# Kernel tuning notes

Hardware: AMD Instinct MI355X
Metric: run time of the kernel (lower is better)

Reference implementation:

```python
import jax, jax.numpy as jnp
import numpy as np

T, B, D = 256, 256, 512
H, DK = 8, 64          # num_heads, d_kv; inner_dim = H*DK = 512
NUM_GROUPS = 16


def setup_inputs() -> dict:
    key = jax.random.key(0)
    ks = jax.random.split(key, 6)
    hidden_states = jax.random.normal(ks[0], (T, B, D), dtype=jnp.float32)
    # sorted group ids over the batch axis (what _infer_group_ids_from_mask recovers)
    group_ids = jnp.sort(jax.random.randint(ks[1], (B,), 0, NUM_GROUPS, dtype=jnp.int32))
    scale = 1.0 / np.sqrt(D)
    Wq = jax.random.normal(ks[2], (D, H * DK), dtype=jnp.float32) * scale
    Wk = jax.random.normal(ks[3], (D, H * DK), dtype=jnp.float32) * scale
    Wv = jax.random.normal(ks[4], (D, H * DK), dtype=jnp.float32) * scale
    Wo = jax.random.normal(ks[5], (H * DK, D), dtype=jnp.float32) * scale
    return {"hidden_states": hidden_states, "group_ids": group_ids,
            "Wq": Wq, "Wk": Wk, "Wv": Wv, "Wo": Wo}


def reference(hidden_states, group_ids, Wq, Wk, Wv, Wo):
    # Group-restricted self-attention along the batch axis, per time step & head.
    # Equivalent to the block-sparse MiniFlash kernel: entries attend only to
    # batch entries with the same group id.
    t, b, d = hidden_states.shape
    q = (hidden_states @ Wq).reshape(t, b, H, DK)
    k = (hidden_states @ Wk).reshape(t, b, H, DK)
    v = (hidden_states @ Wv).reshape(t, b, H, DK)
    sm_scale = 1.0 / np.sqrt(DK)
    # scores: [T, H, B, B] over the batch axis
    scores = jnp.einsum("tihd,tjhd->thij", q, k) * sm_scale
    allowed = group_ids[:, None] == group_ids[None, :]          # [B, B]
    neg = jnp.finfo(scores.dtype).min
    scores = jnp.where(allowed[None, None, :, :], scores, neg)
    attn = jax.nn.softmax(scores, axis=-1)
    out = jnp.einsum("thij,tjhd->tihd", attn, v).reshape(t, b, H * DK)
    return out @ Wo
```

## Files before the change

### kernel.cpp

```cpp
#include <hip/hip_runtime.h>
#include <hip/hip_bf16.h>

typedef __attribute__((ext_vector_type(8))) short short8;
typedef __attribute__((ext_vector_type(4))) short short4v;
typedef __attribute__((ext_vector_type(4))) float f32x4;

#define MFMA16(a, b, c) __builtin_amdgcn_mfma_f32_16x16x32_bf16(a, b, c, 0, 0, 0)

__device__ __forceinline__ unsigned short f2bf(float f) {
    __hip_bfloat16 h = __float2bfloat16(f);
    union { __hip_bfloat16 h; unsigned short u; } v;
    v.h = h;
    return v.u;
}

__device__ __forceinline__ short8 pack8(float4 a, float4 b) {
    short8 p;
    p[0] = (short)f2bf(a.x); p[1] = (short)f2bf(a.y);
    p[2] = (short)f2bf(a.z); p[3] = (short)f2bf(a.w);
    p[4] = (short)f2bf(b.x); p[5] = (short)f2bf(b.y);
    p[6] = (short)f2bf(b.z); p[7] = (short)f2bf(b.w);
    return p;
}

__global__ __launch_bounds__(256) void wprep(
    const float* __restrict__ Wq, const float* __restrict__ Wk,
    const float* __restrict__ Wv, const float* __restrict__ Wo,
    unsigned short* __restrict__ wt)
{
    __shared__ float tile[64][65];
    const int bid = blockIdx.x;
    const int m = bid >> 6, tb = bid & 63;
    const int kr = (tb >> 3) << 6, nc = (tb & 7) << 6;
    const float* W = (m == 0) ? Wq : (m == 1) ? Wk : (m == 2) ? Wv : Wo;
    const int tid = threadIdx.x;
    for (int i = tid; i < 4096; i += 256)
        tile[i >> 6][i & 63] = W[(size_t)(kr + (i >> 6)) * 512 + nc + (i & 63)];
    __syncthreads();
    unsigned short* dst = wt + (size_t)m * 262144;
    for (int i = tid; i < 4096; i += 256)
        dst[(size_t)(nc + (i >> 6)) * 512 + kr + (i & 63)] = f2bf(tile[i & 63][i >> 6]);
}

__global__ __launch_bounds__(1024, 4) void qkv_attn_mfma(
    const float* __restrict__ hs,
    const int*   __restrict__ gid,
    const float* __restrict__ Wq, const float* __restrict__ Wk,
    const float* __restrict__ Wv,
    const unsigned short* __restrict__ wt,
    unsigned short* __restrict__ abuf,
    float*       __restrict__ out)
{
    __shared__ unsigned short Qs[256][72];
    __shared__ unsigned short Ks[256][72];
    __shared__ unsigned short Vts[64][264];
    __shared__ unsigned short Wts[3][64][40];
    __shared__ unsigned short XPs[256 * 72];
    __shared__ int sgid[256];
    __shared__ int glo[16], ghi[16];

    const int bid = blockIdx.x;
    const int h   = (bid & 63) >> 3;
    const int t   = ((bid >> 6) << 3) + (bid & 7);

    const int tid  = threadIdx.x;
    const int lane = tid & 63;
    const int w    = tid >> 6;
    const int l15  = lane & 15;
    const int hi4  = lane >> 4;
    const int wrow = w << 4;

    if (tid < 16) { glo[tid] = 256; ghi[tid] = -1; }
    __syncthreads();
    if (tid < 256) {
        const int g = gid[tid];
        sgid[tid] = g;
        atomicMin(&glo[g], tid);
        atomicMax(&ghi[g], tid);
    }

    const float* __restrict__ Xbase = hs + (size_t)t * (256 * 512);

    f32x4 acc[3][4];
    #pragma unroll
    for (int m = 0; m < 3; ++m)
        #pragma unroll
        for (int n = 0; n < 4; ++n)
            acc[m][n] = (f32x4){0.f, 0.f, 0.f, 0.f};

    const int xi = tid >> 2, xq = tid & 3;
    const bool doW = tid < 768;
    const int wrh = tid >> 2;
    const int wq  = tid & 3;
    const int wm  = wrh >> 6;
    const int wn  = wrh & 63;
    const float* __restrict__ Wsl = (wm == 0) ? Wq : (wm == 1) ? Wk : Wv;

    float4 xf0, xf1;
    short8 wreg;
    {
        const float* s = Xbase + (size_t)xi * 512 + xq * 8;
        xf0 = *(const float4*)s; xf1 = *(const float4*)(s + 4);
        if (doW) {
            if (wt) {
                wreg = *(const short8*)(wt + ((size_t)wm * 512 + h * 64 + wn) * 512 + wq * 8);
            } else {
                #pragma unroll
                for (int j = 0; j < 8; ++j)
                    wreg[j] = (short)f2bf(Wsl[(size_t)(wq * 8 + j) * 512 + h * 64 + wn]);
            }
        }
    }

    for (int kb = 0; kb < 512; kb += 32) {
        *(short8*)&XPs[xi * 40 + xq * 8] = pack8(xf0, xf1);
        if (doW) *(short8*)&Wts[wm][wn][wq * 8] = wreg;
        __syncthreads();
        if (kb < 480) {
            const int kn = kb + 32;
            const float* s = Xbase + (size_t)xi * 512 + kn + xq * 8;
            xf0 = *(const float4*)s; xf1 = *(const float4*)(s + 4);
            if (doW) {
                if (wt) {
                    wreg = *(const short8*)(wt + ((size_t)wm * 512 + h * 64 + wn) * 512 + kn + wq * 8);
                } else {
                    #pragma unroll
                    for (int j = 0; j < 8; ++j)
                        wreg[j] = (short)f2bf(Wsl[(size_t)(kn + wq * 8 + j) * 512 + h * 64 + wn]);
                }
            }
        }
        const short8 af = *(const short8*)&XPs[(wrow + l15) * 40 + hi4 * 8];
        __builtin_amdgcn_s_setprio(1);
        #pragma unroll
        for (int m = 0; m < 3; ++m) {
            #pragma unroll
            for (int n = 0; n < 4; ++n) {
                const short8 bf = *(const short8*)&Wts[m][n * 16 + l15][hi4 * 8];
                acc[m][n] = MFMA16(af, bf, acc[m][n]);
            }
        }
        __builtin_amdgcn_s_setprio(0);
        __syncthreads();
    }

    #pragma unroll
    for (int n = 0; n < 4; ++n) {
        short4v vv;
        #pragma unroll
        for (int r = 0; r < 4; ++r) {
            const int row = wrow + hi4 * 4 + r;
            const int col = n * 16 + l15;
            Qs[row][col] = f2bf(acc[0][n][r]);
            Ks[row][col] = f2bf(acc[1][n][r]);
            vv[r] = (short)f2bf(acc[2][n][r]);
        }
        *(short4v*)&Vts[n * 16 + l15][wrow + hi4 * 4] = vv;
    }
    __syncthreads();

    int rg[4];
    #pragma unroll
    for (int r = 0; r < 4; ++r) rg[r] = sgid[wrow + hi4 * 4 + r];
    const int klo = glo[sgid[wrow]];
    const int khi = ghi[sgid[wrow + 15]];

    short8 qf[2];
    #pragma unroll
    for (int ks = 0; ks < 2; ++ks)
        qf[ks] = *(const short8*)&Qs[wrow + l15][ks * 32 + hi4 * 8];

    f32x4 o[4];
    float mrun[4], lrun[4];
    #pragma unroll
    for (int n = 0; n < 4; ++n) o[n] = (f32x4){0.f, 0.f, 0.f, 0.f};
    #pragma unroll
    for (int r = 0; r < 4; ++r) { mrun[r] = -3.0e38f; lrun[r] = 0.f; }

    for (int kc = klo & ~63; kc <= khi; kc += 64) {
        f32x4 sfr[4];
        __builtin_amdgcn_s_setprio(1);
        #pragma unroll
        for (int n = 0; n < 4; ++n) {
            const int krow = kc + n * 16 + l15;
            const short8 kf0 = *(const short8*)&Ks[krow][hi4 * 8];
            const short8 kf1 = *(const short8*)&Ks[krow][32 + hi4 * 8];
            f32x4 z = (f32x4){0.f, 0.f, 0.f, 0.f};
            z = MFMA16(qf[0], kf0, z);
            z = MFMA16(qf[1], kf1, z);
            sfr[n] = z;
        }
        __builtin_amdgcn_s_setprio(0);
        int cg[4];
        #pragma unroll
        for (int n = 0; n < 4; ++n) cg[n] = sgid[kc + n * 16 + l15];

        #pragma unroll
        for (int r = 0; r < 4; ++r) {
            const int gr = rg[r];
            float sv[4];
            float smax = -3.0e38f;
            #pragma unroll
            for (int n = 0; n < 4; ++n) {
                float x = sfr[n][r] * 0.125f;
                x = (cg[n] == gr) ? x : -3.0e38f;
                sv[n] = x;
                smax = fmaxf(smax, x);
            }
            smax = fmaxf(smax, __shfl_xor(smax, 1));
            smax = fmaxf(smax, __shfl_xor(smax, 2));
            smax = fmaxf(smax, __shfl_xor(smax, 4));
            smax = fmaxf(smax, __shfl_xor(smax, 8));
            const float newm = fmaxf(mrun[r], smax);
            const float corr = __expf(mrun[r] - newm);
            float ps = 0.f;
            unsigned short pb[4];
            #pragma unroll
            for (int n = 0; n < 4; ++n) {
                const float p = (sv[n] > -1.0e38f) ? __expf(sv[n] - newm) : 0.f;
                ps += p;
                pb[n] = f2bf(p);
            }
            ps += __shfl_xor(ps, 1); ps += __shfl_xor(ps, 2);
            ps += __shfl_xor(ps, 4); ps += __shfl_xor(ps, 8);
            lrun[r] = lrun[r] * corr + ps;
            mrun[r] = newm;
            #pragma unroll
            for (int n = 0; n < 4; ++n) o[n][r] *= corr;
            const int prow = wrow + hi4 * 4 + r;
            #pragma unroll
            for (int n = 0; n < 4; ++n)
                XPs[prow * 72 + n * 16 + l15] = pb[n];
        }

        const short8 pa0 = *(const short8*)&XPs[(wrow + l15) * 72 + hi4 * 8];
        const short8 pa1 = *(const short8*)&XPs[(wrow + l15) * 72 + 32 + hi4 * 8];
        __builtin_amdgcn_s_setprio(1);
        #pragma unroll
        for (int n = 0; n < 4; ++n) {
            const short8 vb0 = *(const short8*)&Vts[n * 16 + l15][kc + hi4 * 8];
            const short8 vb1 = *(const short8*)&Vts[n * 16 + l15][kc + 32 + hi4 * 8];
            o[n] = MFMA16(pa0, vb0, o[n]);
            o[n] = MFMA16(pa1, vb1, o[n]);
        }
        __builtin_amdgcn_s_setprio(0);
    }

    if (abuf) {
        unsigned short* __restrict__ op = abuf + (size_t)t * (256 * 512) + h * 64;
        #pragma unroll
        for (int r = 0; r < 4; ++r) {
            const int row = wrow + hi4 * 4 + r;
            const float inv = 1.0f / lrun[r];
            #pragma unroll
            for (int n = 0; n < 4; ++n)
                op[(size_t)row * 512 + n * 16 + l15] = f2bf(o[n][r] * inv);
        }
    } else {
        float* __restrict__ op = out + (size_t)t * (256 * 512) + h * 64;
        #pragma unroll
        for (int r = 0; r < 4; ++r) {
            const int row = wrow + hi4 * 4 + r;
            const float inv = 1.0f / lrun[r];
            #pragma unroll
            for (int n = 0; n < 4; ++n)
                op[(size_t)row * 512 + n * 16 + l15] = o[n][r] * inv;
        }
    }
}

__global__ __launch_bounds__(1024, 4) void oproj_mfma(
    const float* __restrict__ Wo,
    const unsigned short* __restrict__ wot,
    const unsigned short* __restrict__ abuf,
    float* __restrict__ out)
{
    __shared__ unsigned short As[128 * 40];
    __shared__ unsigned short Bts[512 * 40];

    const int tid  = threadIdx.x;
    const int lane = tid & 63;
    const int w    = tid >> 6;
    const int l15  = lane & 15;
    const int hi4  = lane >> 4;
    const int wr   = w >> 2;
    const int wc   = w & 3;
    const size_t r0 = (size_t)blockIdx.x * 128;

    f32x4 acc[2][8];
    #pragma unroll
    for (int m = 0; m < 2; ++m)
        #pragma unroll
        for (int n = 0; n < 8; ++n)
            acc[m][n] = (f32x4){0.f, 0.f, 0.f, 0.f};

    const bool isA = tid < 512;
    const int bn = tid & 511;
    const int ai = bn >> 2, aq = bn & 3;

    float4 af0, af1;
    short8 a8;
    short8 b8[4];

    if (isA) {
        if (abuf) {
            a8 = *(const short8*)(abuf + (r0 + ai) * 512 + aq * 8);
        } else {
            const float* s = out + (r0 + ai) * 512 + aq * 8;
            af0 = *(const float4*)s; af1 = *(const float4*)(s + 4);
        }
    } else {
        if (wot) {
            #pragma unroll
            for (int q = 0; q < 4; ++q)
                b8[q] = *(const short8*)(wot + (size_t)bn * 512 + q * 8);
        } else {
            #pragma unroll
            for (int q = 0; q < 4; ++q)
                #pragma unroll
                for (int j = 0; j < 8; ++j)
                    b8[q][j] = (short)f2bf(Wo[(size_t)(q * 8 + j) * 512 + bn]);
        }
    }

    for (int kb = 0; kb < 512; kb += 32) {
        if (isA) *(short8*)&As[ai * 40 + aq * 8] = abuf ? a8 : pack8(af0, af1);
        else {
            #pragma unroll
            for (int q = 0; q < 4; ++q)
                *(short8*)&Bts[bn * 40 + q * 8] = b8[q];
        }
        __syncthreads();
        if (kb < 480) {
            const int kn = kb + 32;
            if (isA) {
                if (abuf) {
                    a8 = *(const short8*)(abuf + (r0 + ai) * 512 + kn + aq * 8);
                } else {
                    const float* s = out + (r0 + ai) * 512 + kn + aq * 8;
                    af0 = *(const float4*)s; af1 = *(const float4*)(s + 4);
                }
            } else {
                if (wot) {
                    #pragma unroll
                    for (int q = 0; q < 4; ++q)
                        b8[q] = *(const short8*)(wot + (size_t)bn * 512 + kn + q * 8);
                } else {
                    #pragma unroll
                    for (int q = 0; q < 4; ++q)
                        #pragma unroll
                        for (int j = 0; j < 8; ++j)
                            b8[q][j] = (short)f2bf(Wo[(size_t)(kn + q * 8 + j) * 512 + bn]);
                }
            }
        }
        short8 afr[2];
        #pragma unroll
        for (int m = 0; m < 2; ++m)
            afr[m] = *(const short8*)&As[(wr * 32 + m * 16 + l15) * 40 + hi4 * 8];
        __builtin_amdgcn_s_setprio(1);
        #pragma unroll
        for (int n = 0; n < 8; ++n) {
            const short8 bfr = *(const short8*)&Bts[(wc * 128 + n * 16 + l15) * 40 + hi4 * 8];
            #pragma unroll
            for (int m = 0; m < 2; ++m)
                acc[m][n] = MFMA16(afr[m], bfr, acc[m][n]);
        }
        __builtin_amdgcn_s_setprio(0);
        __syncthreads();
    }

    #pragma unroll
    for (int m = 0; m < 2; ++m)
        #pragma unroll
        for (int n = 0; n < 8; ++n)
            #pragma unroll
            for (int r = 0; r < 4; ++r)
                out[(r0 + wr * 32 + m * 16 + hi4 * 4 + r) * 512 + wc * 128 + n * 16 + l15] =
                    acc[m][n][r];
}

extern "C" void kernel_launch(void* const* d_in, const int* in_sizes, int n_in,
                              void* d_out, int out_size, void* d_ws, size_t ws_size,
                              hipStream_t stream) {
    const float* hs  = (const float*)d_in[0];
    const int*   gid = (const int*)  d_in[1];
    const float* Wq  = (const float*)d_in[2];
    const float* Wk  = (const float*)d_in[3];
    const float* Wv  = (const float*)d_in[4];
    const float* Wo  = (const float*)d_in[5];
    float* outp = (float*)d_out;

    const size_t WT_SHORTS = (size_t)4 * 512 * 512;
    const size_t AB_SHORTS = (size_t)256 * 256 * 512;
    unsigned short* wt   = nullptr;
    unsigned short* wot  = nullptr;
    unsigned short* abuf = nullptr;
    if (ws_size >= WT_SHORTS * 2) {
        wt  = (unsigned short*)d_ws;
        wot = wt + (size_t)3 * 512 * 512;
        wprep<<<256, 256, 0, stream>>>(Wq, Wk, Wv, Wo, wt);
        if (ws_size >= (WT_SHORTS + AB_SHORTS) * 2)
            abuf = wt + WT_SHORTS;
    }

    qkv_attn_mfma<<<2048, 1024, 0, stream>>>(hs, gid, Wq, Wk, Wv, wt, abuf, outp);
    oproj_mfma<<<512, 1024, 0, stream>>>(Wo, wot, abuf, outp);
}
```

Baseline: 338.6 us.

## Retile QKV projection with 64x48 warp tiles, XOR-swizzled LDS, drop bf16 abuf

The QKV projection moves from 16-row-per-wave tiles with K-step 32 to 64x48 per-wave tiles with K-step 64, so each loaded A/B fragment feeds more MFMAs and fewer barriers are needed. All LDS tiles switch from padded layouts to XOR-swizzled 64/256-wide layouts to avoid bank conflicts, and the Q tile now reuses the P buffer. The bf16 intermediate attention buffer is removed, so attention writes fp32 to the output and the O-projection reads fp32 and converts it. That doubles intermediate traffic in exchange for simpler code and less workspace.

```diff
diff --git a/kernel.cpp b/kernel.cpp
--- a/kernel.cpp
+++ b/kernel.cpp
@@ -8,9 +8,8 @@
 #define MFMA16(a, b, c) __builtin_amdgcn_mfma_f32_16x16x32_bf16(a, b, c, 0, 0, 0)
 
 __device__ __forceinline__ unsigned short f2bf(float f) {
-    __hip_bfloat16 h = __float2bfloat16(f);
     union { __hip_bfloat16 h; unsigned short u; } v;
-    v.h = h;
+    v.h = __float2bfloat16(f);
     return v.u;
 }
 
@@ -21,6 +20,13 @@
     p[4] = (short)f2bf(b.x); p[5] = (short)f2bf(b.y);
     p[6] = (short)f2bf(b.z); p[7] = (short)f2bf(b.w);
     return p;
+}
+
+__device__ __forceinline__ int swz64(int row, int bytecol) {
+    return row * 64 + ((bytecol ^ ((row & 7) << 4)) >> 1);
+}
+__device__ __forceinline__ int swz256(int row, int bytecol) {
+    return row * 256 + ((bytecol ^ ((row & 7) << 4)) >> 1);
 }
 
 __global__ __launch_bounds__(256) void wprep(
@@ -48,14 +54,13 @@
     const float* __restrict__ Wq, const float* __restrict__ Wk,
     const float* __restrict__ Wv,
     const unsigned short* __restrict__ wt,
-    unsigned short* __restrict__ abuf,
     float*       __restrict__ out)
 {
-    __shared__ unsigned short Qs[256][72];
-    __shared__ unsigned short Ks[256][72];
-    __shared__ unsigned short Vts[64][264];
-    __shared__ unsigned short Wts[3][64][40];
-    __shared__ unsigned short XPs[256 * 72];
+    __shared__ unsigned short Xs[256 * 64];
+    __shared__ unsigned short Wsh[192 * 64];
+    __shared__ unsigned short Ksh[256 * 64];
+    __shared__ unsigned short Vt[64 * 256];
+    __shared__ unsigned short XP[256 * 64];
     __shared__ int sgid[256];
     __shared__ int glo[16], ghi[16];
 
@@ -68,7 +73,8 @@
     const int w    = tid >> 6;
     const int l15  = lane & 15;
     const int hi4  = lane >> 4;
-    const int wrow = w << 4;
+    const int mg   = w & 3;
+    const int ng   = w >> 2;
 
     if (tid < 16) { glo[tid] = 256; ghi[tid] = -1; }
     __syncthreads();
@@ -81,84 +87,119 @@
 
     const float* __restrict__ Xbase = hs + (size_t)t * (256 * 512);
 
-    f32x4 acc[3][4];
-    #pragma unroll
-    for (int m = 0; m < 3; ++m)
-        #pragma unroll
-        for (int n = 0; n < 4; ++n)
-            acc[m][n] = (f32x4){0.f, 0.f, 0.f, 0.f};
-
-    const int xi = tid >> 2, xq = tid & 3;
+    const int xr = tid >> 2, xq = tid & 3;
     const bool doW = tid < 768;
-    const int wrh = tid >> 2;
-    const int wq  = tid & 3;
-    const int wm  = wrh >> 6;
-    const int wn  = wrh & 63;
-    const float* __restrict__ Wsl = (wm == 0) ? Wq : (wm == 1) ? Wk : Wv;
-
-    float4 xf0, xf1;
-    short8 wreg;
+    const int wc = tid >> 2;
+    const int wq = tid & 3;
+    const int wmat = wc >> 6, wcol = wc & 63;
+    const unsigned short* __restrict__ wsrc =
+        wt ? wt + ((size_t)wmat * 512 + h * 64 + wcol) * 512 : nullptr;
+    const float* __restrict__ wfsrc =
+        (wmat == 0) ? Wq : (wmat == 1) ? Wk : Wv;
+
+    f32x4 acc[4][3];
+    #pragma unroll
+    for (int mt = 0; mt < 4; ++mt)
+        #pragma unroll
+        for (int nt = 0; nt < 3; ++nt)
+            acc[mt][nt] = (f32x4){0.f, 0.f, 0.f, 0.f};
+
+    float4 xf[4];
+    short8 w8[2];
     {
-        const float* s = Xbase + (size_t)xi * 512 + xq * 8;
-        xf0 = *(const float4*)s; xf1 = *(const float4*)(s + 4);
+        const float* s = Xbase + (size_t)xr * 512 + xq * 16;
+        xf[0] = *(const float4*)(s + 0);  xf[1] = *(const float4*)(s + 4);
+        xf[2] = *(const float4*)(s + 8);  xf[3] = *(const float4*)(s + 12);
         if (doW) {
             if (wt) {
-                wreg = *(const short8*)(wt + ((size_t)wm * 512 + h * 64 + wn) * 512 + wq * 8);
+                w8[0] = *(const short8*)(wsrc + wq * 16);
+                w8[1] = *(const short8*)(wsrc + wq * 16 + 8);
             } else {
                 #pragma unroll
-                for (int j = 0; j < 8; ++j)
-                    wreg[j] = (short)f2bf(Wsl[(size_t)(wq * 8 + j) * 512 + h * 64 + wn]);
-            }
-        }
-    }
-
-    for (int kb = 0; kb < 512; kb += 32) {
-        *(short8*)&XPs[xi * 40 + xq * 8] = pack8(xf0, xf1);
-        if (doW) *(short8*)&Wts[wm][wn][wq * 8] = wreg;
+                for (int b = 0; b < 2; ++b)
+                    #pragma unroll
+                    for (int j = 0; j < 8; ++j)
+                        w8[b][j] = (short)f2bf(
+                            wfsrc[(size_t)(wq * 16 + b * 8 + j) * 512 + h * 64 + wcol]);
+            }
+        }
+    }
+
+    for (int kb = 0; kb < 512; kb += 64) {
+        *(short8*)&Xs[swz64(xr, xq * 32 + 0)]  = pack8(xf[0], xf[1]);
+        *(short8*)&Xs[swz64(xr, xq * 32 + 16)] = pack8(xf[2], xf[3]);
+        if (doW) {
+            *(short8*)&Wsh[swz64(wc, wq * 32 + 0)]  = w8[0];
+            *(short8*)&Wsh[swz64(wc, wq * 32 + 16)] = w8[1];
+        }
         __syncthreads();
-        if (kb < 480) {
-            const int kn = kb + 32;
-            const float* s = Xbase + (size_t)xi * 512 + kn + xq * 8;
-            xf0 = *(const float4*)s; xf1 = *(const float4*)(s + 4);
+        if (kb < 448) {
+            const int kn = kb + 64;
+            const float* s = Xbase + (size_t)xr * 512 + kn + xq * 16;
+            xf[0] = *(const float4*)(s + 0);  xf[1] = *(const float4*)(s + 4);
+            xf[2] = *(const float4*)(s + 8);  xf[3] = *(const float4*)(s + 12);
             if (doW) {
                 if (wt) {
-                    wreg = *(const short8*)(wt + ((size_t)wm * 512 + h * 64 + wn) * 512 + kn + wq * 8);
+                    w8[0] = *(const short8*)(wsrc + kn + wq * 16);
+                    w8[1] = *(const short8*)(wsrc + kn + wq * 16 + 8);
                 } else {
                     #pragma unroll
-                    for (int j = 0; j < 8; ++j)
-                        wreg[j] = (short)f2bf(Wsl[(size_t)(kn + wq * 8 + j) * 512 + h * 64 + wn]);
+                    for (int b = 0; b < 2; ++b)
+                        #pragma unroll
+                        for (int j = 0; j < 8; ++j)
+                            w8[b][j] = (short)f2bf(
+                                wfsrc[(size_t)(kn + wq * 16 + b * 8 + j) * 512 + h * 64 + wcol]);
                 }
             }
         }
-        const short8 af = *(const short8*)&XPs[(wrow + l15) * 40 + hi4 * 8];
-        __builtin_amdgcn_s_setprio(1);
-        #pragma unroll
-        for (int m = 0; m < 3; ++m) {
-            #pragma unroll
-            for (int n = 0; n < 4; ++n) {
-                const short8 bf = *(const short8*)&Wts[m][n * 16 + l15][hi4 * 8];
-                acc[m][n] = MFMA16(af, bf, acc[m][n]);
-            }
-        }
-        __builtin_amdgcn_s_setprio(0);
+        #pragma unroll
+        for (int ks = 0; ks < 2; ++ks) {
+            short8 af[4];
+            #pragma unroll
+            for (int mt = 0; mt < 4; ++mt)
+                af[mt] = *(const short8*)&Xs[swz64(mg * 64 + mt * 16 + l15,
+                                                   ks * 64 + hi4 * 16)];
+            __builtin_amdgcn_s_setprio(1);
+            #pragma unroll
+            for (int nt = 0; nt < 3; ++nt) {
+                const short8 bf = *(const short8*)&Wsh[swz64(ng * 48 + nt * 16 + l15,
+                                                             ks * 64 + hi4 * 16)];
+                #pragma unroll
+                for (int mt = 0; mt < 4; ++mt)
+                    acc[mt][nt] = MFMA16(af[mt], bf, acc[mt][nt]);
+            }
+            __builtin_amdgcn_s_setprio(0);
+        }
         __syncthreads();
     }
 
     #pragma unroll
-    for (int n = 0; n < 4; ++n) {
-        short4v vv;
-        #pragma unroll
-        for (int r = 0; r < 4; ++r) {
-            const int row = wrow + hi4 * 4 + r;
-            const int col = n * 16 + l15;
-            Qs[row][col] = f2bf(acc[0][n][r]);
-            Ks[row][col] = f2bf(acc[1][n][r]);
-            vv[r] = (short)f2bf(acc[2][n][r]);
-        }
-        *(short4v*)&Vts[n * 16 + l15][wrow + hi4 * 4] = vv;
+    for (int nt = 0; nt < 3; ++nt) {
+        const int c0 = (ng * 3 + nt) * 16;
+        const int m  = c0 >> 6;
+        const int d0 = c0 & 63;
+        #pragma unroll
+        for (int mt = 0; mt < 4; ++mt) {
+            const int rowb = mg * 64 + mt * 16 + hi4 * 4;
+            if (m == 0) {
+                #pragma unroll
+                for (int r = 0; r < 4; ++r)
+                    XP[swz64(rowb + r, (d0 + l15) * 2)] = f2bf(acc[mt][nt][r]);
+            } else if (m == 1) {
+                #pragma unroll
+                for (int r = 0; r < 4; ++r)
+                    Ksh[swz64(rowb + r, (d0 + l15) * 2)] = f2bf(acc[mt][nt][r]);
+            } else {
+                short4v vv;
+                #pragma unroll
+                for (int r = 0; r < 4; ++r) vv[r] = (short)f2bf(acc[mt][nt][r]);
+                *(short4v*)&Vt[swz256(d0 + l15, rowb * 2)] = vv;
+            }
+        }
     }
     __syncthreads();
 
+    const int wrow = w << 4;
     int rg[4];
     #pragma unroll
     for (int r = 0; r < 4; ++r) rg[r] = sgid[wrow + hi4 * 4 + r];
@@ -168,7 +209,7 @@
     short8 qf[2];
     #pragma unroll
     for (int ks = 0; ks < 2; ++ks)
-        qf[ks] = *(const short8*)&Qs[wrow + l15][ks * 32 + hi4 * 8];
+        qf[ks] = *(const short8*)&XP[swz64(wrow + l15, ks * 64 + hi4 * 16)];
 
     f32x4 o[4];
     float mrun[4], lrun[4];
@@ -183,8 +224,8 @@
         #pragma unroll
         for (int n = 0; n < 4; ++n) {
             const int krow = kc + n * 16 + l15;
-            const short8 kf0 = *(const short8*)&Ks[krow][hi4 * 8];
-            const short8 kf1 = *(const short8*)&Ks[krow][32 + hi4 * 8];
+            const short8 kf0 = *(const short8*)&Ksh[swz64(krow, hi4 * 16)];
+            const short8 kf1 = *(const short8*)&Ksh[swz64(krow, 64 + hi4 * 16)];
             f32x4 z = (f32x4){0.f, 0.f, 0.f, 0.f};
             z = MFMA16(qf[0], kf0, z);
             z = MFMA16(qf[1], kf1, z);
@@ -230,49 +271,36 @@
             const int prow = wrow + hi4 * 4 + r;
             #pragma unroll
             for (int n = 0; n < 4; ++n)
-                XPs[prow * 72 + n * 16 + l15] = pb[n];
-        }
-
-        const short8 pa0 = *(const short8*)&XPs[(wrow + l15) * 72 + hi4 * 8];
-        const short8 pa1 = *(const short8*)&XPs[(wrow + l15) * 72 + 32 + hi4 * 8];
+                XP[swz64(prow, (n * 16 + l15) * 2)] = pb[n];
+        }
+
+        const short8 pa0 = *(const short8*)&XP[swz64(wrow + l15, hi4 * 16)];
+        const short8 pa1 = *(const short8*)&XP[swz64(wrow + l15, 64 + hi4 * 16)];
         __builtin_amdgcn_s_setprio(1);
         #pragma unroll
         for (int n = 0; n < 4; ++n) {
-            const short8 vb0 = *(const short8*)&Vts[n * 16 + l15][kc + hi4 * 8];
-            const short8 vb1 = *(const short8*)&Vts[n * 16 + l15][kc + 32 + hi4 * 8];
+            const short8 vb0 = *(const short8*)&Vt[swz256(n * 16 + l15, (kc + hi4 * 8) * 2)];
+            const short8 vb1 = *(const short8*)&Vt[swz256(n * 16 + l15, (kc + 32 + hi4 * 8) * 2)];
             o[n] = MFMA16(pa0, vb0, o[n]);
             o[n] = MFMA16(pa1, vb1, o[n]);
         }
         __builtin_amdgcn_s_setprio(0);
     }
 
-    if (abuf) {
-        unsigned short* __restrict__ op = abuf + (size_t)t * (256 * 512) + h * 64;
-        #pragma unroll
-        for (int r = 0; r < 4; ++r) {
-            const int row = wrow + hi4 * 4 + r;
-            const float inv = 1.0f / lrun[r];
-            #pragma unroll
-            for (int n = 0; n < 4; ++n)
-                op[(size_t)row * 512 + n * 16 + l15] = f2bf(o[n][r] * inv);
-        }
-    } else {
-        float* __restrict__ op = out + (size_t)t * (256 * 512) + h * 64;
-        #pragma unroll
-        for (int r = 0; r < 4; ++r) {
-            const int row = wrow + hi4 * 4 + r;
-            const float inv = 1.0f / lrun[r];
-            #pragma unroll
-            for (int n = 0; n < 4; ++n)
-                op[(size_t)row * 512 + n * 16 + l15] = o[n][r] * inv;
-        }
+    float* __restrict__ op = out + (size_t)t * (256 * 512) + h * 64;
+    #pragma unroll
+    for (int r = 0; r < 4; ++r) {
+        const int row = wrow + hi4 * 4 + r;
+        const float inv = 1.0f / lrun[r];
+        #pragma unroll
+        for (int n = 0; n < 4; ++n)
+            op[(size_t)row * 512 + n * 16 + l15] = o[n][r] * inv;
     }
 }
 
 __global__ __launch_bounds__(1024, 4) void oproj_mfma(
     const float* __restrict__ Wo,
     const unsigned short* __restrict__ wot,
-    const unsigned short* __restrict__ abuf,
     float* __restrict__ out)
 {
     __shared__ unsigned short As[128 * 40];
@@ -299,16 +327,11 @@
     const int ai = bn >> 2, aq = bn & 3;
 
     float4 af0, af1;
-    short8 a8;
     short8 b8[4];
 
     if (isA) {
-        if (abuf) {
-            a8 = *(const short8*)(abuf + (r0 + ai) * 512 + aq * 8);
-        } else {
-            const float* s = out + (r0 + ai) * 512 + aq * 8;
-            af0 = *(const float4*)s; af1 = *(const float4*)(s + 4);
-        }
+        const float* s = out + (r0 + ai) * 512 + aq * 8;
+        af0 = *(const float4*)s; af1 = *(const float4*)(s + 4);
     } else {
         if (wot) {
             #pragma unroll
@@ -324,7 +347,7 @@
     }
 
     for (int kb = 0; kb < 512; kb += 32) {
-        if (isA) *(short8*)&As[ai * 40 + aq * 8] = abuf ? a8 : pack8(af0, af1);
+        if (isA) *(short8*)&As[ai * 40 + aq * 8] = pack8(af0, af1);
         else {
             #pragma unroll
             for (int q = 0; q < 4; ++q)
@@ -334,12 +357,8 @@
         if (kb < 480) {
             const int kn = kb + 32;
             if (isA) {
-                if (abuf) {
-                    a8 = *(const short8*)(abuf + (r0 + ai) * 512 + kn + aq * 8);
-                } else {
-                    const float* s = out + (r0 + ai) * 512 + kn + aq * 8;
-                    af0 = *(const float4*)s; af1 = *(const float4*)(s + 4);
-                }
+                const float* s = out + (r0 + ai) * 512 + kn + aq * 8;
+                af0 = *(const float4*)s; af1 = *(const float4*)(s + 4);
             } else {
                 if (wot) {
                     #pragma unroll
@@ -391,19 +410,14 @@
     const float* Wo  = (const float*)d_in[5];
     float* outp = (float*)d_out;
 
-    const size_t WT_SHORTS = (size_t)4 * 512 * 512;
-    const size_t AB_SHORTS = (size_t)256 * 256 * 512;
-    unsigned short* wt   = nullptr;
-    unsigned short* wot  = nullptr;
-    unsigned short* abuf = nullptr;
-    if (ws_size >= WT_SHORTS * 2) {
+    unsigned short* wt  = nullptr;
+    unsigned short* wot = nullptr;
+    if (ws_size >= (size_t)4 * 512 * 512 * 2) {
         wt  = (unsigned short*)d_ws;
         wot = wt + (size_t)3 * 512 * 512;
         wprep<<<256, 256, 0, stream>>>(Wq, Wk, Wv, Wo, wt);
-        if (ws_size >= (WT_SHORTS + AB_SHORTS) * 2)
-            abuf = wt + WT_SHORTS;
-    }
-
-    qkv_attn_mfma<<<2048, 1024, 0, stream>>>(hs, gid, Wq, Wk, Wv, wt, abuf, outp);
-    oproj_mfma<<<512, 1024, 0, stream>>>(Wo, wot, abuf, outp);
-}
+    }
+
+    qkv_attn_mfma<<<2048, 1024, 0, stream>>>(hs, gid, Wq, Wk, Wv, wt, outp);
+    oproj_mfma<<<512, 1024, 0, stream>>>(Wo, wot, outp);
+}
```

Result: faster. 318.1 us (-6.1%).
